# Kernel optimization log

Hardware: AMD Instinct MI355X
Metric: run time of the kernel (lower is better)

## Reference

```python
import jax, jax.numpy as jnp
import numpy as np

DIM = 1024; SD = 1024; N_BANDS = 4; MIMO_P = 8; BATCH = 2; L = 2048
LOG10000 = float(np.log(10000.0))


def _hippo_freqs(sd):
    n = jnp.arange(sd, dtype=jnp.float32)
    f = jnp.sqrt(2.0 * n + 1.0)
    f = f / f[-1]
    return jnp.exp(-f * LOG10000)


def setup_inputs() -> dict:
    key = jax.random.key(0)
    ks = jax.random.split(key, 16)
    dim, sd = DIM, SD
    wscale = 1.0 / np.sqrt(dim)
    n = jnp.arange(sd, dtype=jnp.float32)
    b0 = jnp.sqrt(2.0 * n + 1.0); b0 = b0 / b0[-1]
    b0_inv = jnp.log(jnp.expm1(jnp.clip(b0, 1e-6, None)))  # softplus^-1 of hippo b
    G = sd // MIMO_P
    inp = dict(
        x=jax.random.normal(ks[0], (BATCH, L, dim), jnp.float32),
        z_prev=jax.random.normal(ks[1], (BATCH, L, dim), jnp.float32),
        W_psi=jax.random.normal(ks[2], (2 * sd, dim), jnp.float32) * wscale,
        b_psi=jnp.zeros(2 * sd, jnp.float32),
        W_phi=jax.random.normal(ks[3], (2 * sd, dim), jnp.float32) * wscale,
        b_phi=jnp.zeros(2 * sd, jnp.float32),
        W_gate=jax.random.normal(ks[4], (1, dim), jnp.float32) * wscale,
        b_gate=jnp.zeros(1, jnp.float32),
        surprise_gain=jnp.zeros(1, jnp.float32),
        omega=_hippo_freqs(sd),
        log_gamma=jax.random.normal(ks[5], (sd,), jnp.float32) * 0.5 - 7.0,
        dt=jnp.float32(np.log(np.expm1(0.1))),  # layer_idx=0, depth=1 -> target_dt=0.1
        W_bs=jax.random.normal(ks[6], (sd, dim), jnp.float32) * 0.02,
        b_bs=b0_inv,
        W_ps=jax.random.uniform(ks[7], (sd, dim), jnp.float32, -wscale, wscale),
        b_ps=jnp.zeros(sd, jnp.float32),
        W_btx=jax.random.normal(ks[8], (sd, dim), jnp.float32) * 0.02,
        b_btx=b0_inv,
        W_bth=jax.random.normal(ks[9], (sd, 2 * sd), jnp.float32) * 0.02,
        b_bth=jnp.zeros(sd, jnp.float32),
        W_ptx=jax.random.uniform(ks[10], (sd, dim), jnp.float32, -wscale, wscale),
        b_ptx=jnp.zeros(sd, jnp.float32),
        mimo_w=jnp.eye(MIMO_P, dtype=jnp.float32)[None].repeat(G, 0)
               + 0.02 * jax.random.normal(ks[11], (G, MIMO_P, MIMO_P), jnp.float32),
        tau=jnp.ones(1, jnp.float32),
        beta=jnp.zeros(1, jnp.float32),
    )
    return inp


def _forward(x, z_prev, W_psi, b_psi, W_phi, b_phi, W_gate, b_gate, surprise_gain,
             omega, log_gamma, dt, W_bs, b_bs, W_ps, b_ps, W_btx, b_btx,
             W_bth, b_bth, W_ptx, b_ptx, mimo_w, tau, beta):
    Bsz, Ls, D = x.shape
    sd = omega.shape[0]
    n_fft = 1 << (2 * Ls - 1).bit_length()  # static

    # unitary mask: band 0 = lowest hippo frequencies (slowest modes) stay lossless
    freqs = _hippo_freqs(sd)
    order = jnp.argsort(freqs)
    band0 = order[: sd // N_BANDS]
    not_unitary = jnp.ones(sd, jnp.float32).at[band0].set(0.0)

    lin = lambda a, W, bb: a @ W.T + bb

    psi_raw = lin(x, W_psi, b_psi)
    psi = jax.lax.complex(psi_raw[..., :sd], psi_raw[..., sd:])
    phi_raw = lin(x, W_phi, b_phi)
    phi = jax.lax.complex(phi_raw[..., :sd], phi_raw[..., sd:])

    gate = jax.nn.sigmoid(lin(x, W_gate, b_gate))  # [B,L,1]
    surprise = jnp.mean(jnp.abs(x - z_prev), -1, keepdims=True)
    gate = gate * (1.0 + jnp.tanh(surprise_gain) * surprise)

    dt_eff = jax.nn.softplus(dt)
    gamma_eff = jax.nn.softplus(log_gamma) * not_unitary
    lam = jax.lax.complex(-gamma_eff, omega)  # [SD]
    t = jnp.arange(Ls, dtype=jnp.float32)
    kernel_raw = jnp.exp(lam[None, :] * (t[:, None] * dt_eff))  # [L,SD] A^t
    k_pad = jnp.concatenate([jnp.zeros((2, sd), kernel_raw.dtype), kernel_raw], 0)
    kernel_simpson = (k_pad[2:] + 4.0 * k_pad[1:-1] + k_pad[:-2]) / 6.0  # Simpson taps

    Kf_scout = jnp.fft.fft(kernel_raw.T, n=n_fft, axis=1)      # [SD,n_fft]
    Kf_true = jnp.fft.fft(kernel_simpson.T, n=n_fft, axis=1)

    def fftconv(U, Kf):  # causal conv via FFT: U [B,L,SD] complex
        Uf = jnp.fft.fft(jnp.transpose(U, (0, 2, 1)), n=n_fft, axis=2)
        H = jnp.fft.ifft(Uf * Kf[None], axis=2)[:, :, :Ls]
        return jnp.transpose(H, (0, 2, 1))

    # ---- scout wave: input-only LTI ----
    b_scout = jax.nn.softplus(lin(x, W_bs, b_bs))
    ph_s = jnp.pi * jnp.tanh(lin(x, W_ps, b_ps))
    Bc_s = jax.lax.complex(b_scout * jnp.cos(ph_s), b_scout * jnp.sin(ph_s))
    U_scout = gate * Bc_s * psi
    H_scout = fftconv(U_scout, Kf_scout)
    H_prev = jnp.pad(H_scout, ((0, 0), (1, 0), (0, 0)))[:, :-1]  # shift by 1
    scout_rms = jnp.sqrt(jnp.mean(H_prev.real ** 2 + H_prev.imag ** 2, -1, keepdims=True) + 1e-6)
    Hn = H_prev / scout_rms
    H_flat = jnp.concatenate([Hn.real, Hn.imag], -1)  # [B,L,2SD]

    # ---- true wave: state-dependent B, Simpson quadrature kernel ----
    b_true = jax.nn.softplus(lin(x, W_btx, b_btx) + lin(H_flat, W_bth, b_bth))
    ph_t = jnp.pi * jnp.tanh(lin(x, W_ptx, b_ptx))
    Bc_t = jax.lax.complex(b_true * jnp.cos(ph_t), b_true * jnp.sin(ph_t))
    U_true = gate * Bc_t * psi
    H = fftconv(U_true, Kf_true)

    read_rms = jnp.sqrt(jnp.mean(H.real ** 2 + H.imag ** 2, -1, keepdims=True) + 1e-6)
    Hn2 = H / read_rms

    # block-diagonal MIMO mixing in groups of mimo_p
    G = sd // MIMO_P
    Hg = Hn2.reshape(Bsz, Ls, G, MIMO_P)
    Hm = jnp.einsum('blgp,gpq->blgq', Hg, mimo_w.astype(Hg.dtype)).reshape(Bsz, Ls, sd)

    # Born-rule measurement: out = Re(h * phi^*), affine read temperature
    out = jnp.real(Hm * jnp.conj(phi))
    return tau * out + beta  # SD == dim -> out_proj is Identity


def reference(x, z_prev, W_psi, b_psi, W_phi, b_phi, W_gate, b_gate, surprise_gain,
              omega, log_gamma, dt, W_bs, b_bs, W_ps, b_ps, W_btx, b_btx,
              W_bth, b_bth, W_ptx, b_ptx, mimo_w, tau, beta):
    return _forward(x, z_prev, W_psi, b_psi, W_phi, b_phi, W_gate, b_gate,
                    surprise_gain, omega, log_gamma, dt, W_bs, b_bs, W_ps, b_ps,
                    W_btx, b_btx, W_bth, b_bth, W_ptx, b_ptx, mimo_w, tau, beta)
```

## Files before the change

### kernel.cpp

```cpp
#include <hip/hip_runtime.h>
#include <math.h>

#define DIMX   1024
#define SDN    1024
#define BATCHN 2
#define LSEQ   2048
#define BLROWS (BATCHN*LSEQ)
#define NCHUNK 64
#define LCHUNK (LSEQ/NCHUNK)
#define PI_F   3.14159265358979f

typedef unsigned short ushort_t;
typedef unsigned int uint_t;
typedef __bf16 bf16_t;
typedef bf16_t bf16x8 __attribute__((ext_vector_type(8)));
typedef float f32x4 __attribute__((ext_vector_type(4)));

__device__ __forceinline__ ushort_t f2bf_rne(float f) {
  unsigned u = __float_as_uint(f);
  u = u + 0x7fffu + ((u >> 16) & 1u);
  return (ushort_t)(u >> 16);
}

__device__ __forceinline__ float bf2f(ushort_t u) {
  return __uint_as_float(((unsigned)u) << 16);
}

__device__ __forceinline__ uint_t pk2(float2 v) {
  return (uint_t)f2bf_rne(v.x) | ((uint_t)f2bf_rne(v.y) << 16);
}
__device__ __forceinline__ float2 upk2(uint_t u) {
  return make_float2(__uint_as_float(u << 16), __uint_as_float(u & 0xffff0000u));
}

__device__ __forceinline__ float2 cfma2(float2 a, float2 v, float2 u) {
  float re = fmaf(a.x, v.x, fmaf(-a.y, v.y, u.x));
  float im = fmaf(a.x, v.y, fmaf(a.y, v.x, u.y));
  return make_float2(re, im);
}

__device__ __forceinline__ float fast_softplus(float x) {
  return x > 15.f ? x : __logf(1.f + __expf(x));
}
__device__ __forceinline__ float fast_tanh(float x) {
  float xc = fminf(fmaxf(x, -9.f), 9.f);
  float t = __expf(2.f * xc);
  return (t - 1.f) * __builtin_amdgcn_rcpf(t + 1.f);
}

__device__ __forceinline__ void gload_lds16(const ushort_t* g, ushort_t* l) {
  __builtin_amdgcn_global_load_lds(
      (const __attribute__((address_space(1))) void*)g,
      (__attribute__((address_space(3))) void*)l, 16, 0, 0);
}

__global__ __launch_bounds__(256) void prep_kernel(
    const float* __restrict__ x, const float* __restrict__ z_prev,
    const float* __restrict__ Wpsi, const float* __restrict__ Wphi,
    const float* __restrict__ Wbs, const float* __restrict__ Wps,
    const float* __restrict__ Wbtx, const float* __restrict__ Wptx,
    const float* __restrict__ Wbth,
    const float* __restrict__ b_psi, const float* __restrict__ b_phi,
    const float* __restrict__ b_bs, const float* __restrict__ b_ps,
    const float* __restrict__ b_btx, const float* __restrict__ b_ptx,
    const float* __restrict__ Wg, const float* __restrict__ bg,
    const float* __restrict__ sg,
    const float* __restrict__ omega, const float* __restrict__ log_gamma,
    const float* __restrict__ dt,
    ushort_t* __restrict__ xb, ushort_t* __restrict__ wcat,
    ushort_t* __restrict__ wbthb, float* __restrict__ bcat,
    float* __restrict__ gate, float2* __restrict__ a_out,
    float2* __restrict__ A_out) {
  int b = blockIdx.x;
  int tid = threadIdx.x;
  if (b < 4096) {
    int i = tid * 4;
    const float* xp = x + (size_t)b * DIMX;
    const float* zp = z_prev + (size_t)b * DIMX;
    float4 xv = *(const float4*)(xp + i);
    float4 zv = *(const float4*)(zp + i);
    float4 wv = *(const float4*)(Wg + i);
    ushort4 o;
    o.x = f2bf_rne(xv.x); o.y = f2bf_rne(xv.y);
    o.z = f2bf_rne(xv.z); o.w = f2bf_rne(xv.w);
    *(ushort4*)(xb + (size_t)b * DIMX + i) = o;
    float dot = xv.x * wv.x + xv.y * wv.y + xv.z * wv.z + xv.w * wv.w;
    float sur = fabsf(xv.x - zv.x) + fabsf(xv.y - zv.y) +
                fabsf(xv.z - zv.z) + fabsf(xv.w - zv.w);
    __shared__ float sdot[256], ssur[256];
    sdot[tid] = dot; ssur[tid] = sur;
    __syncthreads();
    for (int o_ = 128; o_ > 0; o_ >>= 1) {
      if (tid < o_) { sdot[tid] += sdot[tid + o_]; ssur[tid] += ssur[tid + o_]; }
      __syncthreads();
    }
    if (tid == 0) {
      float gs = 1.f / (1.f + expf(-(sdot[0] + bg[0])));
      gate[b] = gs * (1.f + tanhf(sg[0]) * (ssur[0] * (1.f / DIMX)));
    }
    return;
  }
  b -= 4096;
  if (b < 10240) {
    const float* src; ushort_t* dst; int off;
    if (b < 2048)       { src = Wpsi; dst = wcat;             off = b; }
    else if (b < 4096)  { src = Wphi; dst = wcat + 2097152u;  off = b - 2048; }
    else if (b < 5120)  { src = Wbs;  dst = wcat + 4194304u;  off = b - 4096; }
    else if (b < 6144)  { src = Wps;  dst = wcat + 5242880u;  off = b - 5120; }
    else if (b < 7168)  { src = Wbtx; dst = wcat + 6291456u;  off = b - 6144; }
    else if (b < 8192)  { src = Wptx; dst = wcat + 7340032u;  off = b - 7168; }
    else                { src = Wbth; dst = wbthb;            off = b - 8192; }
    int i = (off * 256 + tid) * 4;
    float4 v = *(const float4*)(src + i);
    ushort4 o;
    o.x = f2bf_rne(v.x); o.y = f2bf_rne(v.y);
    o.z = f2bf_rne(v.z); o.w = f2bf_rne(v.w);
    *(ushort4*)(dst + i) = o;
    return;
  }
  b -= 10240;
  if (b < 32) {
    int n = b * 256 + tid;
    float v;
    if (n < 2048) v = b_psi[n];
    else if (n < 4096) v = b_phi[n - 2048];
    else if (n < 5120) v = b_bs[n - 4096];
    else if (n < 6144) v = b_ps[n - 5120];
    else if (n < 7168) v = b_btx[n - 6144];
    else v = b_ptx[n - 7168];
    bcat[n] = v;
    return;
  }
  int s = (b - 32) * 256 + tid;
  double dtv = (double)dt[0];
  double dte = dtv > 20.0 ? dtv : log1p(exp(dtv));
  double gam = 0.0;
  if (s < SDN - SDN / 4) {
    double lg = (double)log_gamma[s];
    gam = lg > 20.0 ? lg : log1p(exp(lg));
  }
  double th = (double)omega[s] * dte;
  double r  = exp(-gam * dte);
  a_out[s] = make_float2((float)(r * cos(th)), (float)(r * sin(th)));
  double thl = th * (double)LCHUNK;
  double rl  = exp(-gam * dte * (double)LCHUNK);
  A_out[s] = make_float2((float)(rl * cos(thl)), (float)(rl * sin(thl)));
}

template<int MODE>
__global__ __launch_bounds__(256, 2) void gemm_bf16(
    const ushort_t* __restrict__ Xb, const ushort_t* __restrict__ Wb,
    const float* __restrict__ bias, ushort_t* __restrict__ Cb) {
  __shared__ ushort_t As[2][4096];
  __shared__ ushort_t Bs[2][4096];
  const int tid = threadIdx.x;
  const int w = tid >> 6, l = tid & 63;
  int bm, bn, ldx, ldw;
  const ushort_t *Xp, *Wp;
  if (MODE == 0) {
    int b = blockIdx.x;
    int xcd = b & 7, idx = b >> 3;
    int tx = ((xcd & 3) << 4) + (idx & 15);
    int ty = ((xcd >> 2) << 4) + (idx >> 4);
    bm = ty << 7; bn = tx << 7;
    ldx = 1024; ldw = 1024;
    Xp = Xb; Wp = Wb;
  } else {
    bm = blockIdx.y << 7; bn = blockIdx.x << 7;
    ldx = 2048; ldw = 2048;
    Xp = Xb + blockIdx.z * 1024;
    Wp = Wb + blockIdx.z * 1024;
  }
  const int wr = w >> 1, wc = w & 1;

  const int srow = tid >> 2;
  const int c8 = (((tid & 3) - (tid >> 3)) & 3) << 3;
  const ushort_t* ga0 = Xp + (size_t)(bm + srow) * ldx + c8;
  const ushort_t* ga1 = Xp + (size_t)(bm + 64 + srow) * ldx + c8;
  const ushort_t* gb0 = Wp + (size_t)(bn + srow) * ldw + c8;
  const ushort_t* gb1 = Wp + (size_t)(bn + 64 + srow) * ldw + c8;

  f32x4 acc[4][4] = {};
  const int nk = 32;

#define STAGE(buf, kt)                                   \
  do {                                                   \
    gload_lds16(ga0 + (kt), &As[buf][w * 512]);          \
    gload_lds16(ga1 + (kt), &As[buf][2048 + w * 512]);   \
    gload_lds16(gb0 + (kt), &Bs[buf][w * 512]);          \
    gload_lds16(gb1 + (kt), &Bs[buf][2048 + w * 512]);   \
  } while (0)

  STAGE(0, 0);
  __syncthreads();

  const int rl = l & 15, kh = l >> 4;
  const int chunkp = (kh + (rl >> 1)) & 3;
  for (int kt = 0; kt < nk; ++kt) {
    int cur = kt & 1;
    if (kt + 1 < nk) STAGE(cur ^ 1, (kt + 1) * 32);
    const uint4* Af = (const uint4*)As[cur];
    const uint4* Bf = (const uint4*)Bs[cur];
    bf16x8 a[4], b[4];
#pragma unroll
    for (int i = 0; i < 4; ++i)
      a[i] = __builtin_bit_cast(bf16x8, Af[(wr * 64 + i * 16 + rl) * 4 + chunkp]);
#pragma unroll
    for (int j = 0; j < 4; ++j)
      b[j] = __builtin_bit_cast(bf16x8, Bf[(wc * 64 + j * 16 + rl) * 4 + chunkp]);
#pragma unroll
    for (int i = 0; i < 4; ++i)
#pragma unroll
      for (int j = 0; j < 4; ++j)
        acc[i][j] = __builtin_amdgcn_mfma_f32_16x16x32_bf16(a[i], b[j], acc[i][j], 0, 0, 0);
    __syncthreads();
  }
#undef STAGE

#pragma unroll
  for (int i = 0; i < 4; ++i) {
    int mrow = bm + wr * 64 + i * 16 + (l >> 4) * 4;
#pragma unroll
    for (int j = 0; j < 4; ++j) {
      int ncol = bn + wc * 64 + j * 16 + (l & 15);
      if (MODE == 0) {
        float bv = bias[ncol];
#pragma unroll
        for (int r = 0; r < 4; ++r)
          Cb[(size_t)(mrow + r) * 8192 + ncol] = f2bf_rne(acc[i][j][r] + bv);
      } else {
        ushort_t* P = Cb + (size_t)blockIdx.z * (4096u * 1024u);
#pragma unroll
        for (int r = 0; r < 4; ++r)
          P[(size_t)(mrow + r) * 1024 + ncol] = f2bf_rne(acc[i][j][r]);
      }
    }
  }
}


__global__ __launch_bounds__(256) void u_scout(
    const float* __restrict__ gate, const ushort_t* __restrict__ proj,
    uint_t* __restrict__ U) {
  int idx2 = blockIdx.x * 256 + threadIdx.x;
  int m = idx2 >> 9, sp = (idx2 & 511) << 1;
  const ushort_t* pr = proj + ((size_t)m << 13);
  float g = gate[m];
  uint_t bsu = *(const uint_t*)(pr + 4096 + sp);
  uint_t psu = *(const uint_t*)(pr + 5120 + sp);
  uint_t pre = *(const uint_t*)(pr + sp);
  uint_t pim = *(const uint_t*)(pr + 1024 + sp);
  uint_t o[2];
#pragma unroll
  for (int e = 0; e < 2; ++e) {
    float bv = fast_softplus(bf2f((ushort_t)(e ? (bsu >> 16) : (bsu & 0xffff))));
    float ph = PI_F * fast_tanh(bf2f((ushort_t)(e ? (psu >> 16) : (psu & 0xffff))));
    float sph, cph;
    __sincosf(ph, &sph, &cph);
    float br = bv * cph, bi = bv * sph;
    float prf = bf2f((ushort_t)(e ? (pre >> 16) : (pre & 0xffff)));
    float pif = bf2f((ushort_t)(e ? (pim >> 16) : (pim & 0xffff)));
    o[e] = pk2(make_float2(g * (br * prf - bi * pif), g * (br * pif + bi * prf)));
  }
  *(uint2*)(U + ((size_t)m << 10) + sp) = make_uint2(o[0], o[1]);
}

__global__ __launch_bounds__(256) void u_true(
    const float* __restrict__ gate, const ushort_t* __restrict__ proj,
    const ushort_t* __restrict__ P0, const ushort_t* __restrict__ P1,
    const float* __restrict__ b_bth, uint_t* __restrict__ U) {
  int idx2 = blockIdx.x * 256 + threadIdx.x;
  int m = idx2 >> 9, sp = (idx2 & 511) << 1;
  const ushort_t* pr = proj + ((size_t)m << 13);
  float g = gate[m];
  size_t base = ((size_t)m << 10) + sp;
  uint_t btu = *(const uint_t*)(pr + 6144 + sp);
  uint_t ptu = *(const uint_t*)(pr + 7168 + sp);
  uint_t p0u = *(const uint_t*)(P0 + base);
  uint_t p1u = *(const uint_t*)(P1 + base);
  float2 bb = *(const float2*)(b_bth + sp);
  uint_t pre = *(const uint_t*)(pr + sp);
  uint_t pim = *(const uint_t*)(pr + 1024 + sp);
  uint_t o[2];
#pragma unroll
  for (int e = 0; e < 2; ++e) {
    float blv = bf2f((ushort_t)(e ? (btu >> 16) : (btu & 0xffff)))
              + bf2f((ushort_t)(e ? (p0u >> 16) : (p0u & 0xffff)))
              + bf2f((ushort_t)(e ? (p1u >> 16) : (p1u & 0xffff)))
              + (e ? bb.y : bb.x);
    float bv = fast_softplus(blv);
    float ph = PI_F * fast_tanh(bf2f((ushort_t)(e ? (ptu >> 16) : (ptu & 0xffff))));
    float sph, cph;
    __sincosf(ph, &sph, &cph);
    float br = bv * cph, bi = bv * sph;
    float prf = bf2f((ushort_t)(e ? (pre >> 16) : (pre & 0xffff)));
    float pif = bf2f((ushort_t)(e ? (pim >> 16) : (pim & 0xffff)));
    o[e] = pk2(make_float2(g * (br * prf - bi * pif), g * (br * pif + bi * prf)));
  }
  *(uint2*)(U + base) = make_uint2(o[0], o[1]);
}

__global__ __launch_bounds__(256) void scan_stage1(
    const uint_t* __restrict__ U, const float2* __restrict__ a,
    float2* __restrict__ carry) {
  int s = blockIdx.x * 256 + threadIdx.x;
  int c = blockIdx.y, b = blockIdx.z;
  float2 av = a[s];
  float2 V = make_float2(0.f, 0.f);
  const uint_t* Up = U + (size_t)(b * LSEQ + c * LCHUNK) * SDN + s;
#pragma unroll 8
  for (int t = 0; t < LCHUNK; ++t)
    V = cfma2(av, V, upk2(Up[(size_t)t * SDN]));
  carry[(size_t)(b * NCHUNK + c) * SDN + s] = V;
}

__global__ __launch_bounds__(256) void scan_stage2(
    const float2* __restrict__ carry, const float2* __restrict__ A,
    float2* __restrict__ prefix) {
  int s = blockIdx.x * 256 + threadIdx.x;
  int b = blockIdx.z;
  float2 Av = A[s];
  float2 P = make_float2(0.f, 0.f);
#pragma unroll 8
  for (int c = 0; c < NCHUNK; ++c) {
    size_t off = (size_t)(b * NCHUNK + c) * SDN + s;
    prefix[off] = P;
    P = cfma2(Av, P, carry[off]);
  }
}

__global__ __launch_bounds__(256) void scan_stage3(
    const uint_t* __restrict__ U, const float2* __restrict__ a,
    const float2* __restrict__ prefix, uint_t* __restrict__ Vout) {
  int s = blockIdx.x * 256 + threadIdx.x;
  int c = blockIdx.y, b = blockIdx.z;
  float2 av = a[s];
  float2 V = prefix[(size_t)(b * NCHUNK + c) * SDN + s];
  size_t base = (size_t)(b * LSEQ + c * LCHUNK) * SDN + s;
#pragma unroll 8
  for (int t = 0; t < LCHUNK; ++t) {
    V = cfma2(av, V, upk2(U[base + (size_t)t * SDN]));
    Vout[base + (size_t)t * SDN] = pk2(V);
  }
}

__global__ __launch_bounds__(256) void hflat_kernel(
    const uint_t* __restrict__ V, ushort_t* __restrict__ Hflat) {
  int m = blockIdx.x;
  int t = m & (LSEQ - 1);
  float2 v[4];
  float sum = 0.f;
#pragma unroll
  for (int i = 0; i < 4; ++i) {
    int s = threadIdx.x + i * 256;
    float2 vv = make_float2(0.f, 0.f);
    if (t > 0) vv = upk2(V[(size_t)(m - 1) * SDN + s]);
    v[i] = vv;
    sum += vv.x * vv.x + vv.y * vv.y;
  }
  __shared__ float red[256];
  red[threadIdx.x] = sum;
  __syncthreads();
  for (int o = 128; o > 0; o >>= 1) {
    if (threadIdx.x < o) red[threadIdx.x] += red[threadIdx.x + o];
    __syncthreads();
  }
  float inv = 1.0f / sqrtf(red[0] * (1.f / SDN) + 1e-6f);
  ushort_t* hr = Hflat + ((size_t)m << 11);
#pragma unroll
  for (int i = 0; i < 4; ++i) {
    int s = threadIdx.x + i * 256;
    hr[s] = f2bf_rne(v[i].x * inv);
    hr[SDN + s] = f2bf_rne(v[i].y * inv);
  }
}

__global__ __launch_bounds__(256) void final_kernel(
    const uint_t* __restrict__ V, const ushort_t* __restrict__ proj,
    const float* __restrict__ mimo, const float* __restrict__ tau,
    const float* __restrict__ beta, float* __restrict__ out) {
  int bid = blockIdx.x;
  int m = ((bid & 7) << 9) | (bid >> 3);
  int t = m & (LSEQ - 1);
  __shared__ float2 hl[SDN];
  __shared__ float red[256];
  float sum = 0.f;
#pragma unroll
  for (int i = 0; i < 4; ++i) {
    int s = threadIdx.x + i * 256;
    float2 v0 = upk2(V[(size_t)m * SDN + s]);
    float2 v1 = make_float2(0.f, 0.f), v2 = make_float2(0.f, 0.f);
    if (t >= 1) v1 = upk2(V[(size_t)(m - 1) * SDN + s]);
    if (t >= 2) v2 = upk2(V[(size_t)(m - 2) * SDN + s]);
    float2 h = make_float2((v0.x + 4.f * v1.x + v2.x) * (1.f / 6.f),
                           (v0.y + 4.f * v1.y + v2.y) * (1.f / 6.f));
    hl[s] = h;
    sum += h.x * h.x + h.y * h.y;
  }
  red[threadIdx.x] = sum;
  __syncthreads();
  for (int o = 128; o > 0; o >>= 1) {
    if (threadIdx.x < o) red[threadIdx.x] += red[threadIdx.x + o];
    __syncthreads();
  }
  float inv = 1.0f / sqrtf(red[0] * (1.f / SDN) + 1e-6f);
  float tv = tau[0], bv = beta[0];
  const ushort_t* pp = proj + ((size_t)m << 13) + 2048;
#pragma unroll
  for (int i = 0; i < 4; ++i) {
    int s = threadIdx.x + i * 256;
    int g = s >> 3, q = s & 7;
    const float* wp = mimo + (size_t)g * 64 + q;
    float hr = 0.f, hi = 0.f;
#pragma unroll
    for (int p = 0; p < 8; ++p) {
      float wv = wp[p * 8];
      float2 hp = hl[(g << 3) + p];
      hr = fmaf(hp.x, wv, hr);
      hi = fmaf(hp.y, wv, hi);
    }
    hr *= inv; hi *= inv;
    float o1 = hr * bf2f(pp[s]) + hi * bf2f(pp[SDN + s]);
    out[(size_t)m * SDN + s] = tv * o1 + bv;
  }
}

extern "C" void kernel_launch(void* const* d_in, const int* in_sizes, int n_in,
                              void* d_out, int out_size, void* d_ws, size_t ws_size,
                              hipStream_t stream) {
  const float* x      = (const float*)d_in[0];
  const float* z_prev = (const float*)d_in[1];
  const float* W_psi  = (const float*)d_in[2];
  const float* b_psi  = (const float*)d_in[3];
  const float* W_phi  = (const float*)d_in[4];
  const float* b_phi  = (const float*)d_in[5];
  const float* W_gate = (const float*)d_in[6];
  const float* b_gate = (const float*)d_in[7];
  const float* s_gain = (const float*)d_in[8];
  const float* omega  = (const float*)d_in[9];
  const float* log_g  = (const float*)d_in[10];
  const float* dt     = (const float*)d_in[11];
  const float* W_bs   = (const float*)d_in[12];
  const float* b_bs   = (const float*)d_in[13];
  const float* W_ps   = (const float*)d_in[14];
  const float* b_ps   = (const float*)d_in[15];
  const float* W_btx  = (const float*)d_in[16];
  const float* b_btx  = (const float*)d_in[17];
  const float* W_bth  = (const float*)d_in[18];
  const float* b_bth  = (const float*)d_in[19];
  const float* W_ptx  = (const float*)d_in[20];
  const float* b_ptx  = (const float*)d_in[21];
  const float* mimo_w = (const float*)d_in[22];
  const float* tau    = (const float*)d_in[23];
  const float* beta   = (const float*)d_in[24];
  float* out = (float*)d_out;

  float* ws = (float*)d_ws;
  const size_t M1 = 1 << 20;
  ushort_t* proj   = (ushort_t*)ws;
  uint_t*   U      = (uint_t*)(ws + 16 * M1);
  uint_t*   V      = U;
  ushort_t* xb     = (ushort_t*)(ws + 24 * M1);
  ushort_t* wcat   = (ushort_t*)(ws + 26 * M1);
  ushort_t* P0     = wcat;
  ushort_t* P1     = wcat + 4u * 1024u * 1024u;
  ushort_t* wbthb  = (ushort_t*)(ws + 30 * M1);
  ushort_t* hflatB = (ushort_t*)(ws + 31 * M1);
  float*    bcat   = ws + 35 * M1;
  float*    gate   = bcat + 8192;
  float2*   ac     = (float2*)(gate + 4096);
  float2*   Ac     = ac + 1024;
  float2*   carry  = Ac + 1024;
  float2*   prefix = carry + 131072;
  (void)ws_size; (void)in_sizes; (void)n_in; (void)out_size;

  dim3 blk(256);
  dim3 sgrid(SDN / 256, NCHUNK, BATCHN);

  prep_kernel<<<dim3(14372), blk, 0, stream>>>(
      x, z_prev, W_psi, W_phi, W_bs, W_ps, W_btx, W_ptx, W_bth,
      b_psi, b_phi, b_bs, b_ps, b_btx, b_ptx,
      W_gate, b_gate, s_gain, omega, log_g, dt,
      xb, wcat, wbthb, bcat, gate, ac, Ac);

  gemm_bf16<0><<<dim3(2048), blk, 0, stream>>>(xb, wcat, bcat, proj);

  u_scout<<<dim3(BLROWS * SDN / 512), blk, 0, stream>>>(gate, proj, U);
  scan_stage1<<<sgrid, blk, 0, stream>>>(U, ac, carry);
  scan_stage2<<<dim3(SDN / 256, 1, BATCHN), blk, 0, stream>>>(carry, Ac, prefix);
  scan_stage3<<<sgrid, blk, 0, stream>>>(U, ac, prefix, V);

  hflat_kernel<<<dim3(BLROWS), blk, 0, stream>>>(V, hflatB);
  gemm_bf16<1><<<dim3(8, 32, 2), blk, 0, stream>>>(hflatB, wbthb, bcat, P0);

  u_true<<<dim3(BLROWS * SDN / 512), blk, 0, stream>>>(gate, proj, P0, P1, b_bth, U);
  scan_stage1<<<sgrid, blk, 0, stream>>>(U, ac, carry);
  scan_stage2<<<dim3(SDN / 256, 1, BATCHN), blk, 0, stream>>>(carry, Ac, prefix);
  scan_stage3<<<sgrid, blk, 0, stream>>>(U, ac, prefix, V);

  final_kernel<<<dim3(BLROWS), blk, 0, stream>>>(V, proj, mimo_w, tau, beta, out);
}
```

Before: 209.4 us.

## Double scan chunk count and parallelize carry propagation with wave shuffle scan

The chunk count of the three-stage linear recurrence scan doubles, so each chunk is half as long. This gives stage1 and stage3 twice as many blocks and shorter serial chains. The previously serial stage2 carry propagation, which ran on only eight blocks, becomes a per-state-dimension Kogge-Stone scan inside a wavefront using shuffles. Each lane combines two chunks, and the per-chunk decay is squared at each step. The costs are twice as many carry/prefix entries and strided, uncoalesced carry loads in stage2. There are also extra complex multiplies, and repeated squaring of the decay can lose some rounding accuracy.

```diff
diff --git a/kernel.cpp b/kernel.cpp
--- a/kernel.cpp
+++ b/kernel.cpp
@@ -6,7 +6,7 @@
 #define BATCHN 2
 #define LSEQ   2048
 #define BLROWS (BATCHN*LSEQ)
-#define NCHUNK 64
+#define NCHUNK 128
 #define LCHUNK (LSEQ/NCHUNK)
 #define PI_F   3.14159265358979f
 
@@ -37,6 +37,9 @@
   float re = fmaf(a.x, v.x, fmaf(-a.y, v.y, u.x));
   float im = fmaf(a.x, v.y, fmaf(a.y, v.x, u.y));
   return make_float2(re, im);
+}
+__device__ __forceinline__ float2 cmul2(float2 a, float2 b) {
+  return make_float2(a.x * b.x - a.y * b.y, a.x * b.y + a.y * b.x);
 }
 
 __device__ __forceinline__ float fast_softplus(float x) {
@@ -315,18 +318,33 @@
 }
 
 __global__ __launch_bounds__(256) void scan_stage2(
-    const float2* __restrict__ carry, const float2* __restrict__ A,
+    const float2* __restrict__ carry, const float2* __restrict__ Ac,
     float2* __restrict__ prefix) {
-  int s = blockIdx.x * 256 + threadIdx.x;
+  int tid = threadIdx.x;
+  int lane = tid & 63;
+  int s = blockIdx.x * 4 + (tid >> 6);
   int b = blockIdx.z;
-  float2 Av = A[s];
-  float2 P = make_float2(0.f, 0.f);
-#pragma unroll 8
-  for (int c = 0; c < NCHUNK; ++c) {
-    size_t off = (size_t)(b * NCHUNK + c) * SDN + s;
-    prefix[off] = P;
-    P = cfma2(Av, P, carry[off]);
-  }
+  float2 Av = Ac[s];
+  size_t base0 = (size_t)(b * NCHUNK + 2 * lane) * SDN + s;
+  float2 c0 = carry[base0];
+  float2 c1 = carry[base0 + SDN];
+  float2 x = cfma2(Av, c0, c1);
+  float2 M = cmul2(Av, Av);
+#pragma unroll
+  for (int sh = 1; sh < 64; sh <<= 1) {
+    float2 y;
+    y.x = __shfl_up(x.x, sh, 64);
+    y.y = __shfl_up(x.y, sh, 64);
+    if (lane >= sh) x = cfma2(M, y, x);
+    M = cmul2(M, M);
+  }
+  float2 p0;
+  p0.x = __shfl_up(x.x, 1, 64);
+  p0.y = __shfl_up(x.y, 1, 64);
+  if (lane == 0) p0 = make_float2(0.f, 0.f);
+  float2 p1 = cfma2(Av, p0, c0);
+  prefix[base0] = p0;
+  prefix[base0 + SDN] = p1;
 }
 
 __global__ __launch_bounds__(256) void scan_stage3(
@@ -471,11 +489,12 @@
   float2*   ac     = (float2*)(gate + 4096);
   float2*   Ac     = ac + 1024;
   float2*   carry  = Ac + 1024;
-  float2*   prefix = carry + 131072;
+  float2*   prefix = carry + 262144;
   (void)ws_size; (void)in_sizes; (void)n_in; (void)out_size;
 
   dim3 blk(256);
   dim3 sgrid(SDN / 256, NCHUNK, BATCHN);
+  dim3 s2grid(SDN / 4, 1, BATCHN);
 
   prep_kernel<<<dim3(14372), blk, 0, stream>>>(
       x, z_prev, W_psi, W_phi, W_bs, W_ps, W_btx, W_ptx, W_bth,
@@ -487,7 +506,7 @@
 
   u_scout<<<dim3(BLROWS * SDN / 512), blk, 0, stream>>>(gate, proj, U);
   scan_stage1<<<sgrid, blk, 0, stream>>>(U, ac, carry);
-  scan_stage2<<<dim3(SDN / 256, 1, BATCHN), blk, 0, stream>>>(carry, Ac, prefix);
+  scan_stage2<<<s2grid, blk, 0, stream>>>(carry, Ac, prefix);
   scan_stage3<<<sgrid, blk, 0, stream>>>(U, ac, prefix, V);
 
   hflat_kernel<<<dim3(BLROWS), blk, 0, stream>>>(V, hflatB);
@@ -495,7 +514,7 @@
 
   u_true<<<dim3(BLROWS * SDN / 512), blk, 0, stream>>>(gate, proj, P0, P1, b_bth, U);
   scan_stage1<<<sgrid, blk, 0, stream>>>(U, ac, carry);
-  scan_stage2<<<dim3(SDN / 256, 1, BATCHN), blk, 0, stream>>>(carry, Ac, prefix);
+  scan_stage2<<<s2grid, blk, 0, stream>>>(carry, Ac, prefix);
   scan_stage3<<<sgrid, blk, 0, stream>>>(U, ac, prefix, V);
 
   final_kernel<<<dim3(BLROWS), blk, 0, stream>>>(V, proj, mimo_w, tau, beta, out);
```

Measured after the change: 202.5 us, median of 2. 1.03x faster.
